# Kernel optimization log

Hardware: AMD Instinct MI355X
Metric: run time of the kernel (lower is better)

The kernel has to match this reference:

```python
import jax, jax.numpy as jnp
import numpy as np

H = 256
NUM_HEADS = 4
HEAD_DIM = H // NUM_HEADS


def _mlp(x, W1, b1, W2, b2):
    # Linear(2H->H) + ReLU + (dropout=identity in eval) + Linear(H->H)
    h = jax.nn.relu(x @ W1.T + b1)
    return h @ W2.T + b2


def setup_inputs() -> dict:
    key = jax.random.key(0)
    ks = jax.random.split(key, 24)
    s2h = 1.0 / np.sqrt(2 * H)
    sh = 1.0 / np.sqrt(H)
    inp = {
        'qubit_embeddings': jax.random.normal(ks[0], (65536, H), jnp.float32),
        'qpu_embeddings': jax.random.normal(ks[1], (64, H), jnp.float32),
        'gate_embeddings': jax.random.normal(ks[2], (65536, H), jnp.float32),
        'all_embeddings': jax.random.normal(ks[3], (131072, H), jnp.float32),
        'time_table': jax.random.normal(ks[4], (1000, H), jnp.float32),
        'map_W1': jax.random.normal(ks[5], (H, 2 * H), jnp.float32) * s2h,
        'map_b1': jnp.zeros((H,), jnp.float32),
        'map_W2': jax.random.normal(ks[6], (H, H), jnp.float32) * sh,
        'map_b2': jnp.zeros((H,), jnp.float32),
        'sch_W1': jax.random.normal(ks[7], (H, 2 * H), jnp.float32) * s2h,
        'sch_b1': jnp.zeros((H,), jnp.float32),
        'sch_W2': jax.random.normal(ks[8], (H, H), jnp.float32) * sh,
        'sch_b2': jnp.zeros((H,), jnp.float32),
        'qg_W1': jax.random.normal(ks[9], (H, H), jnp.float32) * sh,
        'qg_b1': jnp.zeros((H,), jnp.float32),
        'qg_W2': jax.random.normal(ks[10], (H, H), jnp.float32) * sh,
        'qg_b2': jnp.zeros((H,), jnp.float32),
        'attn_Wq': jax.random.normal(ks[11], (H, H), jnp.float32) * sh,
        'attn_bq': jnp.zeros((H,), jnp.float32),
        'attn_Wk': jax.random.normal(ks[12], (H, H), jnp.float32) * sh,
        'attn_bk': jnp.zeros((H,), jnp.float32),
        'attn_Wv': jax.random.normal(ks[13], (H, H), jnp.float32) * sh,
        'attn_bv': jnp.zeros((H,), jnp.float32),
        'attn_Wo': jax.random.normal(ks[14], (H, H), jnp.float32) * sh,
        'attn_bo': jnp.zeros((H,), jnp.float32),
        'map_qubit': jax.random.randint(ks[15], (131072,), 0, 65536, jnp.int32),
        'map_qpu': jax.random.randint(ks[16], (131072,), 0, 64, jnp.int32),
        'sched_gate': jax.random.randint(ks[17], (131072,), 0, 65536, jnp.int32),
        'sched_time': jax.random.randint(ks[18], (131072,), 0, 1000, jnp.int32),
    }
    return inp


def reference(qubit_embeddings, qpu_embeddings, gate_embeddings, all_embeddings,
              time_table, map_W1, map_b1, map_W2, map_b2,
              sch_W1, sch_b1, sch_W2, sch_b2,
              qg_W1, qg_b1, qg_W2, qg_b2,
              attn_Wq, attn_bq, attn_Wk, attn_bk, attn_Wv, attn_bv,
              attn_Wo, attn_bo,
              map_qubit, map_qpu, sched_gate, sched_time):
    # Vectorized form of the per-action Python loop: gather + concat + MLP.
    map_in = jnp.concatenate([qubit_embeddings[map_qubit], qpu_embeddings[map_qpu]], axis=-1)  # [Nm, 2H]
    map_keys = _mlp(map_in, map_W1, map_b1, map_W2, map_b2)                                    # [Nm, H]
    sch_in = jnp.concatenate([gate_embeddings[sched_gate], time_table[sched_time]], axis=-1)   # [Ns, 2H]
    sch_keys = _mlp(sch_in, sch_W1, sch_b1, sch_W2, sch_b2)                                    # [Ns, H]
    keys = jnp.concatenate([map_keys, sch_keys], axis=0)                                       # [A, H]

    g = all_embeddings.mean(axis=0)                                                            # [H]
    query = jax.nn.relu(g @ qg_W1.T + qg_b1) @ qg_W2.T + qg_b2                                 # [H]

    # MultiheadAttention: batch=1, q_len=1, kv_len=A (dropout=0 in eval, mask all-valid).
    q = (query @ attn_Wq.T + attn_bq).reshape(NUM_HEADS, HEAD_DIM)
    k = (keys @ attn_Wk.T + attn_bk).reshape(-1, NUM_HEADS, HEAD_DIM)
    v = (keys @ attn_Wv.T + attn_bv).reshape(-1, NUM_HEADS, HEAD_DIM)
    scores = jnp.einsum('hd,ahd->ha', q, k) / jnp.sqrt(jnp.asarray(HEAD_DIM, q.dtype))
    w = jax.nn.softmax(scores, axis=-1)                                                        # [heads, A]
    ctx = jnp.einsum('ha,ahd->hd', w, v).reshape(H)
    attn_out = ctx @ attn_Wo.T + attn_bo                                                       # [H]

    action_logits = keys @ attn_out                                                            # [A]
    action_probs = jax.nn.softmax(action_logits, axis=-1)
    return action_probs, action_logits
```

## Files before the change

kernel.cpp:

```cpp
#include <hip/hip_runtime.h>
#include <cstdint>
#include <cstddef>

typedef __bf16 bf16_t;
typedef __bf16 bf16x8 __attribute__((ext_vector_type(8)));
typedef __bf16 bf16x4 __attribute__((ext_vector_type(4)));
typedef float f32x4 __attribute__((ext_vector_type(4)));

#define A_TOTAL 262144
#define NMAP    131072

__global__ __launch_bounds__(256) void k_w1b16(
    const float* __restrict__ mW1, const float* __restrict__ sW1,
    bf16_t* __restrict__ dst) {
  int e = blockIdx.x * 256 + threadIdx.x;
  int slice = e >> 16, idx = e & 65535;
  int n = idx >> 8, k = idx & 255;
  float v;
  switch (slice) {
    case 0:  v = mW1[n * 512 + k]; break;
    case 1:  v = mW1[n * 512 + 256 + k]; break;
    case 2:  v = sW1[n * 512 + k]; break;
    default: v = sW1[n * 512 + 256 + k]; break;
  }
  dst[e] = (bf16_t)v;
}

__global__ __launch_bounds__(256) void k_mean(const float* __restrict__ A,
                                              float* __restrict__ part) {
  int t = threadIdx.x, b = blockIdx.x;
  const float* base = A + (size_t)b * 512 * 256 + t;
  float s = 0.f;
  for (int r = 0; r < 512; ++r) s += base[(size_t)r * 256];
  part[b * 256 + t] = s;
}

__global__ __launch_bounds__(256) void k_front(
    const float* __restrict__ meanPart,
    const float* __restrict__ qgW1, const float* __restrict__ qgb1,
    const float* __restrict__ qgW2, const float* __restrict__ qgb2,
    const float* __restrict__ Wq,  const float* __restrict__ bq,
    const float* __restrict__ Wk,
    const float* __restrict__ mW2, const float* __restrict__ sW2,
    float* __restrict__ qw) {
  __shared__ float g[256], h1[256], qry[256], qv[256];
  __shared__ float qks[4][256];
  int t = threadIdx.x;
  float s = 0.f;
  for (int b = 0; b < 256; ++b) s += meanPart[b * 256 + t];
  g[t] = s * (1.0f / 131072.0f);
  __syncthreads();
  {
    const f32x4* row = (const f32x4*)(qgW1 + (size_t)t * 256);
    float acc = 0.f;
    for (int k = 0; k < 64; ++k) {
      f32x4 w = row[k];
      acc += w[0] * g[4 * k] + w[1] * g[4 * k + 1] + w[2] * g[4 * k + 2] + w[3] * g[4 * k + 3];
    }
    h1[t] = fmaxf(acc + qgb1[t], 0.f);
  }
  __syncthreads();
  {
    const f32x4* row = (const f32x4*)(qgW2 + (size_t)t * 256);
    float acc = 0.f;
    for (int k = 0; k < 64; ++k) {
      f32x4 w = row[k];
      acc += w[0] * h1[4 * k] + w[1] * h1[4 * k + 1] + w[2] * h1[4 * k + 2] + w[3] * h1[4 * k + 3];
    }
    qry[t] = acc + qgb2[t];
  }
  __syncthreads();
  {
    const f32x4* row = (const f32x4*)(Wq + (size_t)t * 256);
    float acc = 0.f;
    for (int k = 0; k < 64; ++k) {
      f32x4 w = row[k];
      acc += w[0] * qry[4 * k] + w[1] * qry[4 * k + 1] + w[2] * qry[4 * k + 2] + w[3] * qry[4 * k + 3];
    }
    qv[t] = acc + bq[t];
  }
  __syncthreads();
  for (int h = 0; h < 4; ++h) {
    float acc = 0.f;
    for (int d = 0; d < 64; ++d) acc += qv[h * 64 + d] * Wk[(size_t)(h * 64 + d) * 256 + t];
    qks[h][t] = acc * 0.125f;
  }
  __syncthreads();
  for (int tab = 0; tab < 2; ++tab) {
    const float* W2 = tab ? sW2 : mW2;
    float acc0 = 0.f, acc1 = 0.f, acc2 = 0.f, acc3 = 0.f;
    for (int n = 0; n < 256; ++n) {
      float wv = W2[(size_t)n * 256 + t];
      acc0 += qks[0][n] * wv;
      acc1 += qks[1][n] * wv;
      acc2 += qks[2][n] * wv;
      acc3 += qks[3][n] * wv;
    }
    float* dst = qw + tab * 1024;
    dst[0 * 256 + t] = acc0;
    dst[1 * 256 + t] = acc1;
    dst[2 * 256 + t] = acc2;
    dst[3 * 256 + t] = acc3;
  }
}

__global__ __launch_bounds__(512, 4) void gemm_direct3(
    const float* __restrict__ A0, int M0, const bf16_t* __restrict__ W0,
    const float* __restrict__ b0, bf16_t* __restrict__ C0, int split,
    const float* __restrict__ A1, int M1, const bf16_t* __restrict__ W1,
    const float* __restrict__ b1, bf16_t* __restrict__ C1) {
  __shared__ __align__(16) bf16_t Xo[128][264];
  int blk = blockIdx.x;
  const float* A; int M; const bf16_t* W; const float* bias; bf16_t* C; int bid;
  if (blk < split) { A = A0; M = M0; W = W0; bias = b0; C = C0; bid = blk; }
  else             { A = A1; M = M1; W = W1; bias = b1; C = C1; bid = blk - split; }
  int t = threadIdx.x;
  int w = t >> 6, lane = t & 63;
  int lm = lane & 15, q = lane >> 4;
  int mloc0 = (w & 1) * 64;
  int m0 = bid * 128 + mloc0;
  int c0 = (w >> 1) * 64;
  int rows[4];
#pragma unroll
  for (int i = 0; i < 4; ++i) {
    int m = m0 + i * 16 + lm;
    rows[i] = m < M ? m : M - 1;
  }
  f32x4 acc[4][4] = {};
#pragma unroll
  for (int kt = 0; kt < 8; ++kt) {
    int k0 = kt * 32 + q * 8;
    bf16x8 b[4];
#pragma unroll
    for (int j = 0; j < 4; ++j)
      b[j] = *(const bf16x8*)(W + (size_t)(c0 + j * 16 + lm) * 256 + k0);
#pragma unroll
    for (int i = 0; i < 4; ++i) {
      const float* src = A + (size_t)rows[i] * 256 + k0;
      f32x4 lo = *(const f32x4*)src;
      f32x4 hi = *(const f32x4*)(src + 4);
      bf16x8 a;
#pragma unroll
      for (int x = 0; x < 4; ++x) { a[x] = (bf16_t)lo[x]; a[x + 4] = (bf16_t)hi[x]; }
#pragma unroll
      for (int j = 0; j < 4; ++j)
        acc[i][j] = __builtin_amdgcn_mfma_f32_16x16x32_bf16(a, b[j], acc[i][j], 0, 0, 0);
    }
  }
#pragma unroll
  for (int j = 0; j < 4; ++j) {
    int col = c0 + j * 16 + lm;
    float bb = bias ? bias[col] : 0.f;
#pragma unroll
    for (int i = 0; i < 4; ++i)
#pragma unroll
      for (int r = 0; r < 4; ++r)
        Xo[mloc0 + i * 16 + q * 4 + r][col] = (bf16_t)(acc[i][j][r] + bb);
  }
  __syncthreads();
  size_t tile0 = (size_t)bid * 128;
  const char* lds = (const char*)&Xo[0][0];
#pragma unroll
  for (int s = 0; s < 8; ++s) {
    int flat = s * 8192 + t * 16;
    int row = flat >> 9, colb = flat & 511;
    if (tile0 + (size_t)row < (size_t)M) {
      uint4 v = *(const uint4*)(lds + row * 528 + colb);
      *(uint4*)((char*)C + tile0 * 512 + (size_t)flat) = v;
    }
  }
}

__global__ __launch_bounds__(256) void k_gx(
    const bf16_t* __restrict__ Pa0, const bf16_t* __restrict__ Pb0,
    const int* __restrict__ idxA0, const int* __restrict__ idxB0,
    const bf16_t* __restrict__ Pa1, const bf16_t* __restrict__ Pb1,
    const int* __restrict__ idxA1, const int* __restrict__ idxB1,
    const float* __restrict__ qw,
    bf16_t* __restrict__ X, float* __restrict__ scores,
    float* __restrict__ partMax) {
  __shared__ float qs[4][256];
  __shared__ float sc[4][64];
  int t = threadIdx.x;
  int b = blockIdx.x;
  int rows0 = b * 64;
  int half = rows0 >= NMAP ? 1 : 0;
  const bf16_t* Pa = half ? Pa1 : Pa0;
  const bf16_t* Pb = half ? Pb1 : Pb0;
  const int* idxA = half ? idxA1 : idxA0;
  const int* idxB = half ? idxB1 : idxB0;
  int lrow0 = rows0 - half * NMAP;

  {
    f32x4 v = *(const f32x4*)(qw + half * 1024 + t * 4);
    *(f32x4*)&((float*)qs)[t * 4] = v;
  }

  int rg = t >> 5;
  int cl = t & 31;
  int ia[8], ib[8];
#pragma unroll
  for (int it = 0; it < 8; ++it) {
    ia[it] = idxA[lrow0 + it * 8 + rg];
    ib[it] = idxB[lrow0 + it * 8 + rg];
  }
  __syncthreads();

#pragma unroll
  for (int it = 0; it < 8; ++it) {
    int rowg = it * 8 + rg;
    bf16x8 a8 = *(const bf16x8*)(Pa + (size_t)ia[it] * 256 + cl * 8);
    bf16x8 b8 = *(const bf16x8*)(Pb + (size_t)ib[it] * 256 + cl * 8);
    float x[8];
    bf16x8 xo;
#pragma unroll
    for (int e = 0; e < 8; ++e) {
      x[e] = fmaxf((float)a8[e] + (float)b8[e], 0.f);
      xo[e] = (bf16_t)x[e];
    }
    *(bf16x8*)(X + (size_t)(rows0 + rowg) * 256 + cl * 8) = xo;
    float p[4] = {0.f, 0.f, 0.f, 0.f};
#pragma unroll
    for (int h = 0; h < 4; ++h)
#pragma unroll
      for (int e = 0; e < 8; ++e)
        p[h] += x[e] * qs[h][cl * 8 + e];
#pragma unroll
    for (int h = 0; h < 4; ++h) {
#pragma unroll
      for (int o = 16; o > 0; o >>= 1) p[h] += __shfl_xor(p[h], o);
      if (cl == 0) sc[h][rowg] = p[h];
    }
  }
  __syncthreads();
  {
    int h = t >> 6, l = t & 63;
    float v = sc[h][l];
    scores[(size_t)h * A_TOTAL + rows0 + l] = v;
    float m = v;
#pragma unroll
    for (int o = 32; o > 0; o >>= 1) m = fmaxf(m, __shfl_xor(m, o));
    if (l == 0) partMax[h * 4096 + b] = m;
  }
}

__global__ __launch_bounds__(256) void k_smax2(const float* __restrict__ pM,
                                               float* __restrict__ Mh) {
  int t = threadIdx.x;
  __shared__ float red[256];
  for (int h = 0; h < 4; ++h) {
    float m = -3.4e38f;
    for (int i = t; i < 4096; i += 256) m = fmaxf(m, pM[h * 4096 + i]);
    red[t] = m;
    __syncthreads();
    for (int s = 128; s > 0; s >>= 1) {
      if (t < s) red[t] = fmaxf(red[t], red[t + s]);
      __syncthreads();
    }
    if (t == 0) Mh[h] = red[0];
    __syncthreads();
  }
}

__global__ __launch_bounds__(256) void k_ssum(const float* __restrict__ scores,
                                              const float* __restrict__ Mh,
                                              float* __restrict__ part) {
  int b = blockIdx.x, t = threadIdx.x;
  float m = Mh[b >> 6];
  const float* base = scores + (size_t)b * 4096;
  float s = 0.f;
  for (int i = 0; i < 16; ++i) s += __expf(base[i * 256 + t] - m);
  __shared__ float red[256];
  red[t] = s;
  __syncthreads();
  for (int st = 128; st > 0; st >>= 1) {
    if (t < st) red[t] += red[t + st];
    __syncthreads();
  }
  if (t == 0) part[b] = red[0];
}

__global__ __launch_bounds__(256) void k_ssum2(const float* __restrict__ part,
                                               float* __restrict__ invS) {
  int t = threadIdx.x;
  __shared__ float red[256];
  red[t] = part[t];
  __syncthreads();
  for (int s = 32; s > 0; s >>= 1) {
    if ((t & 63) < s) red[t] += red[t + s];
    __syncthreads();
  }
  if ((t & 63) == 0) invS[t >> 6] = 1.0f / red[t];
}

__global__ __launch_bounds__(256) void k_u3(
    const bf16_t* __restrict__ X, const float* __restrict__ scores,
    const float* __restrict__ Mh, const float* __restrict__ invS,
    float* __restrict__ y, float* __restrict__ shalf) {
  __shared__ float wl[4][512];
  __shared__ float uloc[8][4][256];
  int t = threadIdx.x;
  int a0 = blockIdx.x * 512;
  int half = blockIdx.x >> 8;
#pragma unroll
  for (int i = 0; i < 8; ++i) {
    int e = i * 256 + t;
    int h = e >> 9, rr = e & 511;
    wl[h][rr] = __expf(scores[(size_t)h * A_TOTAL + a0 + rr] - Mh[h]) * invS[h];
  }
  __syncthreads();
  {
    int h = t >> 6, l = t & 63;
    float s = 0.f;
#pragma unroll
    for (int j = 0; j < 8; ++j) s += wl[h][l + j * 64];
#pragma unroll
    for (int o = 32; o > 0; o >>= 1) s += __shfl_xor(s, o);
    if (l == 0) atomicAdd(&shalf[half * 4 + h], s);
  }
  int tc = t & 31, rh = t >> 5;
  float acc[4][8] = {};
  for (int rr = 0; rr < 64; ++rr) {
    int al = rh * 64 + rr;
    bf16x8 kv = *(const bf16x8*)(X + (size_t)(a0 + al) * 256 + tc * 8);
    float f[8];
#pragma unroll
    for (int e = 0; e < 8; ++e) f[e] = (float)kv[e];
#pragma unroll
    for (int h = 0; h < 4; ++h) {
      float wv = wl[h][al];
#pragma unroll
      for (int e = 0; e < 8; ++e) acc[h][e] += wv * f[e];
    }
  }
#pragma unroll
  for (int h = 0; h < 4; ++h)
#pragma unroll
    for (int e = 0; e < 8; ++e) uloc[rh][h][tc * 8 + e] = acc[h][e];
  __syncthreads();
#pragma unroll
  for (int h = 0; h < 4; ++h) {
    float v = 0.f;
#pragma unroll
    for (int g = 0; g < 8; ++g) v += uloc[g][h][t];
    atomicAdd(&y[(half * 4 + h) * 256 + t], v);
  }
}

__global__ __launch_bounds__(256) void k_attn2(
    const float* __restrict__ y,
    const float* __restrict__ shalf,
    const float* __restrict__ mW2, const float* __restrict__ sW2,
    const float* __restrict__ mb2, const float* __restrict__ sb2,
    const float* __restrict__ Wv, const float* __restrict__ bv,
    const float* __restrict__ Wo, const float* __restrict__ bo,
    float* __restrict__ attnv, float* __restrict__ c01) {
  __shared__ float ys[2][4][256];
  __shared__ float us[4][256];
  __shared__ float ctx[256];
  __shared__ float att[256];
  __shared__ float r0[4], r1[4];
  int t = threadIdx.x;
#pragma unroll
  for (int i = 0; i < 8; ++i) ((float*)ys)[i * 256 + t] = y[i * 256 + t];
  __syncthreads();
  {
    int j = t;
    float a0 = 0.f, a1 = 0.f, a2 = 0.f, a3 = 0.f;
    const f32x4* rm = (const f32x4*)(mW2 + (size_t)j * 256);
    const f32x4* rs = (const f32x4*)(sW2 + (size_t)j * 256);
    for (int k = 0; k < 64; ++k) {
      f32x4 wm = rm[k], wsv = rs[k];
#pragma unroll
      for (int e = 0; e < 4; ++e) {
        float w0 = wm[e], w1 = wsv[e];
        int kk = k * 4 + e;
        a0 += ys[0][0][kk] * w0 + ys[1][0][kk] * w1;
        a1 += ys[0][1][kk] * w0 + ys[1][1][kk] * w1;
        a2 += ys[0][2][kk] * w0 + ys[1][2][kk] * w1;
        a3 += ys[0][3][kk] * w0 + ys[1][3][kk] * w1;
      }
    }
    float bm = mb2[j], bs = sb2[j];
    us[0][j] = a0 + shalf[0] * bm + shalf[4] * bs;
    us[1][j] = a1 + shalf[1] * bm + shalf[5] * bs;
    us[2][j] = a2 + shalf[2] * bm + shalf[6] * bs;
    us[3][j] = a3 + shalf[3] * bm + shalf[7] * bs;
  }
  __syncthreads();
  {
    int h = t >> 6;
    const f32x4* row = (const f32x4*)(Wv + (size_t)t * 256);
    const f32x4* uh = (const f32x4*)us[h];
    float acc = 0.f;
    for (int k = 0; k < 64; ++k) {
      f32x4 w = row[k], x = uh[k];
      acc += w[0] * x[0] + w[1] * x[1] + w[2] * x[2] + w[3] * x[3];
    }
    ctx[t] = acc + bv[t];
  }
  __syncthreads();
  {
    const f32x4* row = (const f32x4*)(Wo + (size_t)t * 256);
    const f32x4* cx = (const f32x4*)ctx;
    float acc = 0.f;
    for (int k = 0; k < 64; ++k) {
      f32x4 w = row[k], x = cx[k];
      acc += w[0] * x[0] + w[1] * x[1] + w[2] * x[2] + w[3] * x[3];
    }
    float v = acc + bo[t];
    att[t] = v;
    attnv[t] = v;
  }
  __syncthreads();
  {
    float p0 = mb2[t] * att[t], p1 = sb2[t] * att[t];
#pragma unroll
    for (int o = 32; o > 0; o >>= 1) {
      p0 += __shfl_xor(p0, o);
      p1 += __shfl_xor(p1, o);
    }
    if ((t & 63) == 0) { r0[t >> 6] = p0; r1[t >> 6] = p1; }
    __syncthreads();
    if (t == 0) c01[0] = r0[0] + r0[1] + r0[2] + r0[3];
    if (t == 1) c01[1] = r1[0] + r1[1] + r1[2] + r1[3];
  }
}

__global__ __launch_bounds__(256) void k_zc(
    const float* __restrict__ mW2, const float* __restrict__ sW2,
    const float* __restrict__ attnv, bf16_t* __restrict__ zpad) {
  int tab = blockIdx.x, t = threadIdx.x;
  const float* W2 = tab ? sW2 : mW2;
  __shared__ float att[256];
  att[t] = attnv[t];
  __syncthreads();
  float acc = 0.f;
  for (int j = 0; j < 256; ++j) acc += W2[(size_t)j * 256 + t] * att[j];
  bf16_t* dst = zpad + (size_t)tab * 16 * 256;
  dst[t] = (bf16_t)acc;
#pragma unroll
  for (int i = 1; i < 16; ++i) dst[i * 256 + t] = (bf16_t)0.f;
}

__global__ __launch_bounds__(256) void k_logits3(
    const bf16_t* __restrict__ X, const bf16_t* __restrict__ zpad,
    const float* __restrict__ c01,
    float* __restrict__ out_logits, float* __restrict__ blockMax) {
  int t = threadIdx.x;
  int w = t >> 6, lane = t & 63;
  int lm = lane & 15, q = lane >> 4;
  int half = blockIdx.x >> 9;
  float c = c01[half];
  int m0 = blockIdx.x * 256 + w * 64;
  const bf16_t* zp = zpad + (size_t)half * 16 * 256;
  bf16x8 b[8];
#pragma unroll
  for (int kt = 0; kt < 8; ++kt)
    b[kt] = *(const bf16x8*)(zp + lm * 256 + kt * 32 + q * 8);
  f32x4 acc[4] = {};
#pragma unroll
  for (int i = 0; i < 4; ++i) {
    const bf16_t* arow = X + (size_t)(m0 + i * 16 + lm) * 256 + q * 8;
#pragma unroll
    for (int kt = 0; kt < 8; ++kt) {
      bf16x8 a = *(const bf16x8*)(arow + kt * 32);
      acc[i] = __builtin_amdgcn_mfma_f32_16x16x32_bf16(a, b[kt], acc[i], 0, 0, 0);
    }
  }
  float lmax = -3.4e38f;
  if (lm == 0) {
#pragma unroll
    for (int i = 0; i < 4; ++i) {
      f32x4 v4;
#pragma unroll
      for (int rr = 0; rr < 4; ++rr) {
        float v = acc[i][rr] + c;
        v4[rr] = v;
        lmax = fmaxf(lmax, v);
      }
      *(f32x4*)(out_logits + m0 + i * 16 + q * 4) = v4;
    }
  }
  float m1 = fmaxf(lmax, __shfl_xor(lmax, 16));
  float m2 = fmaxf(m1, __shfl_xor(m1, 32));
  __shared__ float red[4];
  if (lane == 0) red[w] = m2;
  __syncthreads();
  if (t == 0)
    blockMax[blockIdx.x] = fmaxf(fmaxf(red[0], red[1]), fmaxf(red[2], red[3]));
}

__global__ __launch_bounds__(256) void k_lred1(const float* __restrict__ bm,
                                               float* __restrict__ Ml) {
  int t = threadIdx.x;
  float m = -3.4e38f;
  for (int i = t; i < 1024; i += 256) m = fmaxf(m, bm[i]);
  __shared__ float red[256];
  red[t] = m;
  __syncthreads();
  for (int s = 128; s > 0; s >>= 1) {
    if (t < s) red[t] = fmaxf(red[t], red[t + s]);
    __syncthreads();
  }
  if (t == 0) Ml[0] = red[0];
}

__global__ __launch_bounds__(256) void k_lsum(const float* __restrict__ logits,
                                              const float* __restrict__ Ml,
                                              float* __restrict__ part) {
  int t = threadIdx.x, b = blockIdx.x;
  float m = Ml[0];
  float s = __expf(logits[b * 512 + t] - m) + __expf(logits[b * 512 + 256 + t] - m);
  __shared__ float red[256];
  red[t] = s;
  __syncthreads();
  for (int st = 128; st > 0; st >>= 1) {
    if (t < st) red[t] += red[t + st];
    __syncthreads();
  }
  if (t == 0) part[b] = red[0];
}

__global__ __launch_bounds__(256) void k_lred2(const float* __restrict__ part,
                                               float* __restrict__ invSl) {
  int t = threadIdx.x;
  float s = part[t] + part[t + 256];
  __shared__ float red[256];
  red[t] = s;
  __syncthreads();
  for (int st = 128; st > 0; st >>= 1) {
    if (t < st) red[t] += red[t + st];
    __syncthreads();
  }
  if (t == 0) invSl[0] = 1.0f / red[0];
}

__global__ __launch_bounds__(256) void k_probs(const float* __restrict__ logits,
                                               const float* __restrict__ Ml,
                                               const float* __restrict__ invSl,
                                               float* __restrict__ probs) {
  int i = blockIdx.x * 256 + threadIdx.x;
  probs[i] = __expf(logits[i] - Ml[0]) * invSl[0];
}

extern "C" void kernel_launch(void* const* d_in, const int* in_sizes, int n_in,
                              void* d_out, int out_size, void* d_ws, size_t ws_size,
                              hipStream_t stream) {
  const float* qubit_emb = (const float*)d_in[0];
  const float* qpu_emb   = (const float*)d_in[1];
  const float* gate_emb  = (const float*)d_in[2];
  const float* all_emb   = (const float*)d_in[3];
  const float* time_tab  = (const float*)d_in[4];
  const float* map_W1 = (const float*)d_in[5];
  const float* map_b1 = (const float*)d_in[6];
  const float* map_W2 = (const float*)d_in[7];
  const float* map_b2 = (const float*)d_in[8];
  const float* sch_W1 = (const float*)d_in[9];
  const float* sch_b1 = (const float*)d_in[10];
  const float* sch_W2 = (const float*)d_in[11];
  const float* sch_b2 = (const float*)d_in[12];
  const float* qg_W1 = (const float*)d_in[13];
  const float* qg_b1 = (const float*)d_in[14];
  const float* qg_W2 = (const float*)d_in[15];
  const float* qg_b2 = (const float*)d_in[16];
  const float* Wq = (const float*)d_in[17];
  const float* bq = (const float*)d_in[18];
  const float* Wk = (const float*)d_in[19];
  const float* Wv = (const float*)d_in[21];
  const float* bv = (const float*)d_in[22];
  const float* Wo = (const float*)d_in[23];
  const float* bo = (const float*)d_in[24];
  const int* map_qubit  = (const int*)d_in[25];
  const int* map_qpu    = (const int*)d_in[26];
  const int* sched_gate = (const int*)d_in[27];
  const int* sched_time = (const int*)d_in[28];
  (void)in_sizes; (void)n_in; (void)out_size;

  char* ws = (char*)d_ws;
  size_t off = 0;
  auto alloc = [&](size_t b) { size_t r = off; off += (b + 255) & ~(size_t)255; return r; };
  size_t XB    = alloc((size_t)A_TOTAL * 256 * 2);
  size_t PQ    = alloc((size_t)65536 * 256 * 2);
  size_t PG    = alloc((size_t)65536 * 256 * 2);
  size_t PP    = alloc((size_t)128 * 256 * 2);
  size_t PT    = alloc((size_t)1024 * 256 * 2);
  size_t W1B   = alloc((size_t)4 * 65536 * 2);
  size_t QW    = alloc((size_t)2 * 4 * 256 * 4);
  size_t SCORE = alloc((size_t)4 * A_TOTAL * 4);
  size_t MPART = alloc((size_t)256 * 256 * 4);
  size_t ZPAD  = alloc((size_t)2 * 16 * 256 * 2);
  size_t ATTNV = alloc(256 * 4);
  size_t Y     = alloc(2 * 4 * 256 * 4);
  size_t SH    = alloc(2 * 4 * 4);
  size_t C01   = alloc(2 * 4);
  size_t PMAX  = alloc(4 * 4096 * 4);
  size_t MH    = alloc(4 * 4);
  size_t SINV  = alloc(4 * 4);
  size_t BMAX  = alloc(1024 * 4);
  size_t ML    = alloc(4);
  size_t SLINV = alloc(4);
  size_t LPART = alloc(512 * 4);
  size_t SPART = alloc(256 * 4);
  if (off > ws_size) return;

  bf16_t* xP     = (bf16_t*)(ws + XB);
  bf16_t* pqP    = (bf16_t*)(ws + PQ);
  bf16_t* pgP    = (bf16_t*)(ws + PG);
  bf16_t* ppP    = (bf16_t*)(ws + PP);
  bf16_t* ptP    = (bf16_t*)(ws + PT);
  bf16_t* w1bP   = (bf16_t*)(ws + W1B);
  float*  qwP    = (float*)(ws + QW);
  float*  scoreP = (float*)(ws + SCORE);
  float*  mpartP = (float*)(ws + MPART);
  bf16_t* zpadP  = (bf16_t*)(ws + ZPAD);
  float*  attnvP = (float*)(ws + ATTNV);
  float*  yP     = (float*)(ws + Y);
  float*  shP    = (float*)(ws + SH);
  float*  c01P   = (float*)(ws + C01);
  float*  pmaxP  = (float*)(ws + PMAX);
  float*  mhP    = (float*)(ws + MH);
  float*  sinvP  = (float*)(ws + SINV);
  float*  bmaxP  = (float*)(ws + BMAX);
  float*  mlP    = (float*)(ws + ML);
  float*  slinvP = (float*)(ws + SLINV);
  float*  lpartP = (float*)(ws + LPART);
  float*  spartP = (float*)(ws + SPART);

  float* probsOut  = (float*)d_out;
  float* logitsOut = probsOut + A_TOTAL;

  hipMemsetAsync(yP, 0, 8448, stream);

  k_w1b16<<<1024, 256, 0, stream>>>(map_W1, sch_W1, w1bP);
  k_mean<<<256, 256, 0, stream>>>(all_emb, mpartP);
  k_front<<<1, 256, 0, stream>>>(mpartP, qg_W1, qg_b1, qg_W2, qg_b2,
                                 Wq, bq, Wk, map_W2, sch_W2, qwP);

  gemm_direct3<<<1024, 512, 0, stream>>>(
      qubit_emb, 65536, w1bP + 0 * 65536, nullptr, pqP, 512,
      gate_emb,  65536, w1bP + 2 * 65536, nullptr, pgP);
  gemm_direct3<<<9, 512, 0, stream>>>(
      qpu_emb, 64,   w1bP + 1 * 65536, map_b1, ppP, 1,
      time_tab, 1000, w1bP + 3 * 65536, sch_b1, ptP);

  k_gx<<<4096, 256, 0, stream>>>(
      pqP, ppP, map_qubit, map_qpu,
      pgP, ptP, sched_gate, sched_time,
      qwP, xP, scoreP, pmaxP);

  k_smax2<<<1, 256, 0, stream>>>(pmaxP, mhP);
  k_ssum<<<256, 256, 0, stream>>>(scoreP, mhP, spartP);
  k_ssum2<<<1, 256, 0, stream>>>(spartP, sinvP);

  k_u3<<<512, 256, 0, stream>>>(xP, scoreP, mhP, sinvP, yP, shP);
  k_attn2<<<1, 256, 0, stream>>>(yP, shP, map_W2, sch_W2, map_b2, sch_b2,
                                 Wv, bv, Wo, bo, attnvP, c01P);
  k_zc<<<2, 256, 0, stream>>>(map_W2, sch_W2, attnvP, zpadP);

  k_logits3<<<1024, 256, 0, stream>>>(xP, zpadP, c01P, logitsOut, bmaxP);
  k_lred1<<<1, 256, 0, stream>>>(bmaxP, mlP);
  k_lsum<<<512, 256, 0, stream>>>(logitsOut, mlP, lpartP);
  k_lred2<<<1, 256, 0, stream>>>(lpartP, slinvP);
  k_probs<<<1024, 256, 0, stream>>>(logitsOut, mlP, slinvP, probsOut);
}
```

Before: 717.1 us.

## Parallelize mean reduction and split single-block attention tail into multi-block kernels

The column mean over all_embeddings now uses 2048 blocks with vectorized float4 loads and a two-level reduction (k_mean, then k_mean2), replacing 256 blocks that each did strided scalar loops. The serial single-block k_attn2 and two-block k_zc matrix-vector chains become per-row multi-block kernels (k_u4, k_ctx, k_att, k_z, k_zfin), with atomics accumulating c01. k_gx keeps the query weights in registers instead of staging them in shared memory, which removes a barrier. This adds several kernel launches and atomics, and the memset is widened so that it also zeroes c01.

After: 674.2 us. -6.0%, faster.

```diff
diff --git a/kernel.cpp b/kernel.cpp
--- a/kernel.cpp
+++ b/kernel.cpp
@@ -28,15 +28,33 @@
 
 __global__ __launch_bounds__(256) void k_mean(const float* __restrict__ A,
                                               float* __restrict__ part) {
+  __shared__ f32x4 sred[4][64];
   int t = threadIdx.x, b = blockIdx.x;
-  const float* base = A + (size_t)b * 512 * 256 + t;
+  int cg = t & 63, rs = t >> 6;
+  const float* base = A + ((size_t)b * 64 + rs * 16) * 256 + cg * 4;
+  f32x4 acc = {};
+#pragma unroll
+  for (int r = 0; r < 16; ++r)
+    acc += *(const f32x4*)(base + (size_t)r * 256);
+  sred[rs][cg] = acc;
+  __syncthreads();
+  if (t < 64) {
+    f32x4 tot = sred[0][t] + sred[1][t] + sred[2][t] + sred[3][t];
+    *(f32x4*)(part + (size_t)b * 256 + t * 4) = tot;
+  }
+}
+
+__global__ __launch_bounds__(256) void k_mean2(const float* __restrict__ part,
+                                               float* __restrict__ part2) {
+  int t = threadIdx.x, j = blockIdx.x;
+  const float* base = part + (size_t)j * 128 * 256 + t;
   float s = 0.f;
-  for (int r = 0; r < 512; ++r) s += base[(size_t)r * 256];
-  part[b * 256 + t] = s;
+  for (int i = 0; i < 128; ++i) s += base[(size_t)i * 256];
+  part2[j * 256 + t] = s;
 }
 
 __global__ __launch_bounds__(256) void k_front(
-    const float* __restrict__ meanPart,
+    const float* __restrict__ part2,
     const float* __restrict__ qgW1, const float* __restrict__ qgb1,
     const float* __restrict__ qgW2, const float* __restrict__ qgb2,
     const float* __restrict__ Wq,  const float* __restrict__ bq,
@@ -47,7 +65,8 @@
   __shared__ float qks[4][256];
   int t = threadIdx.x;
   float s = 0.f;
-  for (int b = 0; b < 256; ++b) s += meanPart[b * 256 + t];
+#pragma unroll
+  for (int b = 0; b < 16; ++b) s += part2[b * 256 + t];
   g[t] = s * (1.0f / 131072.0f);
   __syncthreads();
   {
@@ -179,7 +198,6 @@
     const float* __restrict__ qw,
     bf16_t* __restrict__ X, float* __restrict__ scores,
     float* __restrict__ partMax) {
-  __shared__ float qs[4][256];
   __shared__ float sc[4][64];
   int t = threadIdx.x;
   int b = blockIdx.x;
@@ -191,20 +209,20 @@
   const int* idxB = half ? idxB1 : idxB0;
   int lrow0 = rows0 - half * NMAP;
 
-  {
-    f32x4 v = *(const f32x4*)(qw + half * 1024 + t * 4);
-    *(f32x4*)&((float*)qs)[t * 4] = v;
-  }
-
   int rg = t >> 5;
   int cl = t & 31;
+  f32x4 q4[4][2];
+#pragma unroll
+  for (int h = 0; h < 4; ++h) {
+    q4[h][0] = *(const f32x4*)(qw + half * 1024 + h * 256 + cl * 8);
+    q4[h][1] = *(const f32x4*)(qw + half * 1024 + h * 256 + cl * 8 + 4);
+  }
   int ia[8], ib[8];
 #pragma unroll
   for (int it = 0; it < 8; ++it) {
     ia[it] = idxA[lrow0 + it * 8 + rg];
     ib[it] = idxB[lrow0 + it * 8 + rg];
   }
-  __syncthreads();
 
 #pragma unroll
   for (int it = 0; it < 8; ++it) {
@@ -224,7 +242,7 @@
     for (int h = 0; h < 4; ++h)
 #pragma unroll
       for (int e = 0; e < 8; ++e)
-        p[h] += x[e] * qs[h][cl * 8 + e];
+        p[h] += x[e] * q4[h][e >> 2][e & 3];
 #pragma unroll
     for (int h = 0; h < 4; ++h) {
 #pragma unroll
@@ -347,100 +365,99 @@
   }
 }
 
-__global__ __launch_bounds__(256) void k_attn2(
-    const float* __restrict__ y,
-    const float* __restrict__ shalf,
+__global__ __launch_bounds__(256) void k_u4(
+    const float* __restrict__ y, const float* __restrict__ shalf,
     const float* __restrict__ mW2, const float* __restrict__ sW2,
     const float* __restrict__ mb2, const float* __restrict__ sb2,
-    const float* __restrict__ Wv, const float* __restrict__ bv,
-    const float* __restrict__ Wo, const float* __restrict__ bo,
-    float* __restrict__ attnv, float* __restrict__ c01) {
-  __shared__ float ys[2][4][256];
-  __shared__ float us[4][256];
-  __shared__ float ctx[256];
-  __shared__ float att[256];
-  __shared__ float r0[4], r1[4];
-  int t = threadIdx.x;
-#pragma unroll
-  for (int i = 0; i < 8; ++i) ((float*)ys)[i * 256 + t] = y[i * 256 + t];
-  __syncthreads();
-  {
-    int j = t;
-    float a0 = 0.f, a1 = 0.f, a2 = 0.f, a3 = 0.f;
-    const f32x4* rm = (const f32x4*)(mW2 + (size_t)j * 256);
-    const f32x4* rs = (const f32x4*)(sW2 + (size_t)j * 256);
-    for (int k = 0; k < 64; ++k) {
-      f32x4 wm = rm[k], wsv = rs[k];
-#pragma unroll
-      for (int e = 0; e < 4; ++e) {
-        float w0 = wm[e], w1 = wsv[e];
-        int kk = k * 4 + e;
-        a0 += ys[0][0][kk] * w0 + ys[1][0][kk] * w1;
-        a1 += ys[0][1][kk] * w0 + ys[1][1][kk] * w1;
-        a2 += ys[0][2][kk] * w0 + ys[1][2][kk] * w1;
-        a3 += ys[0][3][kk] * w0 + ys[1][3][kk] * w1;
-      }
-    }
-    float bm = mb2[j], bs = sb2[j];
-    us[0][j] = a0 + shalf[0] * bm + shalf[4] * bs;
-    us[1][j] = a1 + shalf[1] * bm + shalf[5] * bs;
-    us[2][j] = a2 + shalf[2] * bm + shalf[6] * bs;
-    us[3][j] = a3 + shalf[3] * bm + shalf[7] * bs;
-  }
-  __syncthreads();
-  {
-    int h = t >> 6;
-    const f32x4* row = (const f32x4*)(Wv + (size_t)t * 256);
-    const f32x4* uh = (const f32x4*)us[h];
-    float acc = 0.f;
-    for (int k = 0; k < 64; ++k) {
-      f32x4 w = row[k], x = uh[k];
-      acc += w[0] * x[0] + w[1] * x[1] + w[2] * x[2] + w[3] * x[3];
-    }
-    ctx[t] = acc + bv[t];
-  }
-  __syncthreads();
-  {
-    const f32x4* row = (const f32x4*)(Wo + (size_t)t * 256);
-    const f32x4* cx = (const f32x4*)ctx;
-    float acc = 0.f;
-    for (int k = 0; k < 64; ++k) {
-      f32x4 w = row[k], x = cx[k];
-      acc += w[0] * x[0] + w[1] * x[1] + w[2] * x[2] + w[3] * x[3];
-    }
-    float v = acc + bo[t];
-    att[t] = v;
-    attnv[t] = v;
-  }
-  __syncthreads();
-  {
-    float p0 = mb2[t] * att[t], p1 = sb2[t] * att[t];
-#pragma unroll
-    for (int o = 32; o > 0; o >>= 1) {
-      p0 += __shfl_xor(p0, o);
-      p1 += __shfl_xor(p1, o);
-    }
-    if ((t & 63) == 0) { r0[t >> 6] = p0; r1[t >> 6] = p1; }
-    __syncthreads();
-    if (t == 0) c01[0] = r0[0] + r0[1] + r0[2] + r0[3];
-    if (t == 1) c01[1] = r1[0] + r1[1] + r1[2] + r1[3];
-  }
-}
-
-__global__ __launch_bounds__(256) void k_zc(
+    float* __restrict__ u) {
+  __shared__ float wsum[4][4];
+  int j = blockIdx.x, t = threadIdx.x;
+  int w = t >> 6, lane = t & 63;
+  float pm = mW2[(size_t)j * 256 + t], ps = sW2[(size_t)j * 256 + t];
+  float p[4];
+#pragma unroll
+  for (int h = 0; h < 4; ++h)
+    p[h] = y[(0 + h) * 256 + t] * pm + y[(4 + h) * 256 + t] * ps;
+#pragma unroll
+  for (int h = 0; h < 4; ++h)
+#pragma unroll
+    for (int o = 32; o > 0; o >>= 1) p[h] += __shfl_xor(p[h], o);
+  if (lane == 0)
+#pragma unroll
+    for (int h = 0; h < 4; ++h) wsum[w][h] = p[h];
+  __syncthreads();
+  if (t < 4) {
+    float tot = wsum[0][t] + wsum[1][t] + wsum[2][t] + wsum[3][t];
+    u[t * 256 + j] = tot + shalf[t] * mb2[j] + shalf[4 + t] * sb2[j];
+  }
+}
+
+__global__ __launch_bounds__(256) void k_ctx(
+    const float* __restrict__ u, const float* __restrict__ Wv,
+    const float* __restrict__ bv, float* __restrict__ ctxv) {
+  __shared__ float wsum[4];
+  int j = blockIdx.x, t = threadIdx.x;
+  int w = t >> 6, lane = t & 63;
+  int h = j >> 6;
+  float p = Wv[(size_t)j * 256 + t] * u[h * 256 + t];
+#pragma unroll
+  for (int o = 32; o > 0; o >>= 1) p += __shfl_xor(p, o);
+  if (lane == 0) wsum[w] = p;
+  __syncthreads();
+  if (t == 0)
+    ctxv[j] = wsum[0] + wsum[1] + wsum[2] + wsum[3] + bv[j];
+}
+
+__global__ __launch_bounds__(256) void k_att(
+    const float* __restrict__ ctxv, const float* __restrict__ Wo,
+    const float* __restrict__ bo,
+    const float* __restrict__ mb2, const float* __restrict__ sb2,
+    float* __restrict__ attv, float* __restrict__ c01) {
+  __shared__ float wsum[4];
+  int j = blockIdx.x, t = threadIdx.x;
+  int w = t >> 6, lane = t & 63;
+  float p = Wo[(size_t)j * 256 + t] * ctxv[t];
+#pragma unroll
+  for (int o = 32; o > 0; o >>= 1) p += __shfl_xor(p, o);
+  if (lane == 0) wsum[w] = p;
+  __syncthreads();
+  if (t == 0) {
+    float a = wsum[0] + wsum[1] + wsum[2] + wsum[3] + bo[j];
+    attv[j] = a;
+    atomicAdd(&c01[0], mb2[j] * a);
+    atomicAdd(&c01[1], sb2[j] * a);
+  }
+}
+
+__global__ __launch_bounds__(256) void k_z(
     const float* __restrict__ mW2, const float* __restrict__ sW2,
-    const float* __restrict__ attnv, bf16_t* __restrict__ zpad) {
-  int tab = blockIdx.x, t = threadIdx.x;
+    const float* __restrict__ attv, float* __restrict__ zpart) {
+  __shared__ float as[16];
+  int b = blockIdx.x, t = threadIdx.x;
+  int tab = b >> 4, jc = b & 15;
   const float* W2 = tab ? sW2 : mW2;
-  __shared__ float att[256];
-  att[t] = attnv[t];
+  if (t < 16) as[t] = attv[jc * 16 + t];
   __syncthreads();
   float acc = 0.f;
-  for (int j = 0; j < 256; ++j) acc += W2[(size_t)j * 256 + t] * att[j];
-  bf16_t* dst = zpad + (size_t)tab * 16 * 256;
-  dst[t] = (bf16_t)acc;
-#pragma unroll
-  for (int i = 1; i < 16; ++i) dst[i * 256 + t] = (bf16_t)0.f;
+#pragma unroll
+  for (int i = 0; i < 16; ++i)
+    acc += as[i] * W2[(size_t)(jc * 16 + i) * 256 + t];
+  zpart[b * 256 + t] = acc;
+}
+
+__global__ __launch_bounds__(256) void k_zfin(
+    const float* __restrict__ zpart, bf16_t* __restrict__ zpad) {
+  int t = threadIdx.x;
+#pragma unroll
+  for (int tab = 0; tab < 2; ++tab) {
+    float s = 0.f;
+#pragma unroll
+    for (int i = 0; i < 16; ++i) s += zpart[(tab * 16 + i) * 256 + t];
+    bf16_t* dst = zpad + (size_t)tab * 16 * 256;
+    dst[t] = (bf16_t)s;
+#pragma unroll
+    for (int i = 1; i < 16; ++i) dst[i * 256 + t] = (bf16_t)0.f;
+  }
 }
 
 __global__ __launch_bounds__(256) void k_logits3(
@@ -588,20 +605,24 @@
   size_t W1B   = alloc((size_t)4 * 65536 * 2);
   size_t QW    = alloc((size_t)2 * 4 * 256 * 4);
   size_t SCORE = alloc((size_t)4 * A_TOTAL * 4);
-  size_t MPART = alloc((size_t)256 * 256 * 4);
+  size_t MPART = alloc((size_t)2048 * 256 * 4);
+  size_t MPRT2 = alloc((size_t)16 * 256 * 4);
   size_t ZPAD  = alloc((size_t)2 * 16 * 256 * 2);
-  size_t ATTNV = alloc(256 * 4);
+  size_t ZPART = alloc((size_t)32 * 256 * 4);
+  size_t U     = alloc(4 * 256 * 4);
+  size_t CTXV  = alloc(256 * 4);
+  size_t ATTV  = alloc(256 * 4);
   size_t Y     = alloc(2 * 4 * 256 * 4);
   size_t SH    = alloc(2 * 4 * 4);
   size_t C01   = alloc(2 * 4);
   size_t PMAX  = alloc(4 * 4096 * 4);
   size_t MH    = alloc(4 * 4);
   size_t SINV  = alloc(4 * 4);
+  size_t SPART = alloc(256 * 4);
   size_t BMAX  = alloc(1024 * 4);
   size_t ML    = alloc(4);
   size_t SLINV = alloc(4);
   size_t LPART = alloc(512 * 4);
-  size_t SPART = alloc(256 * 4);
   if (off > ws_size) return;
 
   bf16_t* xP     = (bf16_t*)(ws + XB);
@@ -613,28 +634,33 @@
   float*  qwP    = (float*)(ws + QW);
   float*  scoreP = (float*)(ws + SCORE);
   float*  mpartP = (float*)(ws + MPART);
+  float*  mprt2P = (float*)(ws + MPRT2);
   bf16_t* zpadP  = (bf16_t*)(ws + ZPAD);
-  float*  attnvP = (float*)(ws + ATTNV);
+  float*  zpartP = (float*)(ws + ZPART);
+  float*  uP     = (float*)(ws + U);
+  float*  ctxvP  = (float*)(ws + CTXV);
+  float*  attvP  = (float*)(ws + ATTV);
   float*  yP     = (float*)(ws + Y);
   float*  shP    = (float*)(ws + SH);
   float*  c01P   = (float*)(ws + C01);
   float*  pmaxP  = (float*)(ws + PMAX);
   float*  mhP    = (float*)(ws + MH);
   float*  sinvP  = (float*)(ws + SINV);
+  float*  spartP = (float*)(ws + SPART);
   float*  bmaxP  = (float*)(ws + BMAX);
   float*  mlP    = (float*)(ws + ML);
   float*  slinvP = (float*)(ws + SLINV);
   float*  lpartP = (float*)(ws + LPART);
-  float*  spartP = (float*)(ws + SPART);
 
   float* probsOut  = (float*)d_out;
   float* logitsOut = probsOut + A_TOTAL;
 
-  hipMemsetAsync(yP, 0, 8448, stream);
+  hipMemsetAsync(yP, 0, 8704, stream);
 
   k_w1b16<<<1024, 256, 0, stream>>>(map_W1, sch_W1, w1bP);
-  k_mean<<<256, 256, 0, stream>>>(all_emb, mpartP);
-  k_front<<<1, 256, 0, stream>>>(mpartP, qg_W1, qg_b1, qg_W2, qg_b2,
+  k_mean<<<2048, 256, 0, stream>>>(all_emb, mpartP);
+  k_mean2<<<16, 256, 0, stream>>>(mpartP, mprt2P);
+  k_front<<<1, 256, 0, stream>>>(mprt2P, qg_W1, qg_b1, qg_W2, qg_b2,
                                  Wq, bq, Wk, map_W2, sch_W2, qwP);
 
   gemm_direct3<<<1024, 512, 0, stream>>>(
@@ -654,9 +680,11 @@
   k_ssum2<<<1, 256, 0, stream>>>(spartP, sinvP);
 
   k_u3<<<512, 256, 0, stream>>>(xP, scoreP, mhP, sinvP, yP, shP);
-  k_attn2<<<1, 256, 0, stream>>>(yP, shP, map_W2, sch_W2, map_b2, sch_b2,
-                                 Wv, bv, Wo, bo, attnvP, c01P);
-  k_zc<<<2, 256, 0, stream>>>(map_W2, sch_W2, attnvP, zpadP);
+  k_u4<<<256, 256, 0, stream>>>(yP, shP, map_W2, sch_W2, map_b2, sch_b2, uP);
+  k_ctx<<<256, 256, 0, stream>>>(uP, Wv, bv, ctxvP);
+  k_att<<<256, 256, 0, stream>>>(ctxvP, Wo, bo, map_b2, sch_b2, attvP, c01P);
+  k_z<<<32, 256, 0, stream>>>(map_W2, sch_W2, attvP, zpartP);
+  k_zfin<<<1, 256, 0, stream>>>(zpartP, zpadP);
 
   k_logits3<<<1024, 256, 0, stream>>>(xP, zpadP, c01P, logitsOut, bmaxP);
   k_lred1<<<1, 256, 0, stream>>>(bmaxP, mlP);
```
